# Performance work log

Hardware: AMD Instinct MI355X
Metric: run time of the kernel (lower is better)

Reference implementation:

```python
import jax, jax.numpy as jnp
import numpy as np

B, N, D = 4, 1024, 1024
H, DH = 16, 64
N_LAYERS = 3  # len(mlp_dims) - 1 with implicit_mlp_hiddens=(64, 64)
EPS = 1.1920929e-07  # torch.nn.RMSNorm default eps = finfo(float32).eps


def _rope_tables(n, dtype):
    # lucidrains RotaryEmbedding: theta=10000, interleaved freq repeat
    inv_freq = 1.0 / (10000.0 ** (np.arange(0, DH, 2, dtype=np.float64) / DH))
    t = np.arange(n, dtype=np.float64)[:, None] * inv_freq[None, :]  # [n, DH/2]
    t = np.repeat(t, 2, axis=-1)  # [n, DH], freqs interleaved (f0,f0,f1,f1,...)
    return jnp.asarray(np.cos(t), dtype), jnp.asarray(np.sin(t), dtype)


def _rope_rotate(x, cos, sin):
    # x: [b,h,n,d]; rotate_half on interleaved pairs: (x1,x2) -> (-x2,x1)
    xp = x.reshape(*x.shape[:-1], DH // 2, 2)
    xr = jnp.stack((-xp[..., 1], xp[..., 0]), axis=-1).reshape(x.shape)
    return x * cos + xr * sin


def _attend(q, k, v):
    # rotate_queries_with_cached_keys with no cache: same positions for q and k
    n = q.shape[-2]
    cos, sin = _rope_tables(n, q.dtype)
    q = _rope_rotate(q, cos, sin)
    k = _rope_rotate(k, cos, sin)
    scale = DH ** -0.5
    scores = jnp.einsum('bhqd,bhkd->bhqk', q, k) * scale
    causal = jnp.tril(jnp.ones((n, n), dtype=bool))
    scores = jnp.where(causal, scores, -jnp.inf)
    attn = jax.nn.softmax(scores, axis=-1)
    return jnp.einsum('bhqk,bhkd->bhqd', attn, v)


def _split_heads(x):
    b, n, _ = x.shape
    return x.reshape(b, n, H, DH).transpose(0, 2, 1, 3)  # b h n d


def setup_inputs() -> dict:
    key = jax.random.key(0)
    ks = jax.random.split(key, 6)
    s = 0.02
    return {
        'tokens': jax.random.normal(ks[0], (B, N, D), jnp.float32),
        'gamma': jnp.ones((D,), jnp.float32),                                  # RMSNorm weight
        'Wq': jax.random.normal(ks[1], (D, H * DH), jnp.float32) * s,           # to_queries
        'Wk': jax.random.normal(ks[2], (N_LAYERS, D, H * DH), jnp.float32) * s, # stacked key projections
        'Wv': jax.random.normal(ks[3], (N_LAYERS, D, H * DH), jnp.float32) * s, # stacked value projections
        'Wo': jax.random.normal(ks[4], (H * DH, D), jnp.float32) * s,           # to_out
    }


def reference(tokens, gamma, Wq, Wk, Wv, Wo):
    b, n, d = tokens.shape
    # RMSNorm (prenorm)
    x = tokens * jax.lax.rsqrt(jnp.mean(tokens * tokens, axis=-1, keepdims=True) + EPS) * gamma
    out = _split_heads(x @ Wq)  # queries, [b h n d]
    for i in range(N_LAYERS):
        k = _split_heads(x @ Wk[i])
        v = _split_heads(x @ Wv[i])
        out = _attend(out, k, v)
        if i < N_LAYERS - 1:
            out = jax.nn.silu(out)  # implicit MLP activation between attention stages
    out = out.transpose(0, 2, 1, 3).reshape(b, n, H * DH)  # merge heads
    return out @ Wo
```

## Files before the change

### kernel.cpp

```cpp
#include <hip/hip_runtime.h>


typedef unsigned short u16;
typedef short s16x8 __attribute__((ext_vector_type(8)));
typedef u16 u16x4 __attribute__((ext_vector_type(4)));
typedef float f32x4 __attribute__((ext_vector_type(4)));

typedef __attribute__((address_space(1))) const unsigned int as1c_uint;
typedef __attribute__((address_space(3))) unsigned int as3_uint;

__device__ __forceinline__ float b2f(u16 h) {
  union { unsigned int u; float f; } v; v.u = ((unsigned int)h) << 16; return v.f;
}
__device__ __forceinline__ u16 f2b(float f) {
  union { float f; unsigned int u; } v; v.f = f;
  return (u16)((v.u + 0x7FFFu + ((v.u >> 16) & 1u)) >> 16);
}
__device__ __forceinline__ void gload16(const u16* g, const u16* lds) {
  __builtin_amdgcn_global_load_lds((as1c_uint*)(size_t)g,
                                   (as3_uint*)(unsigned int)(size_t)lds, 16, 0, 0);
}

__global__ __launch_bounds__(256)
void rmsnorm_kernel(const float* __restrict__ T, const float* __restrict__ gamma,
                    u16* __restrict__ X) {
  const int row = blockIdx.x, tid = threadIdx.x;
  const float4 v = ((const float4*)(T + (size_t)row * 1024))[tid];
  float ss = v.x * v.x + v.y * v.y + v.z * v.z + v.w * v.w;
#pragma unroll
  for (int msk = 1; msk <= 32; msk <<= 1) ss += __shfl_xor(ss, msk, 64);
  __shared__ float red[4];
  if ((tid & 63) == 0) red[tid >> 6] = ss;
  __syncthreads();
  const float tot = red[0] + red[1] + red[2] + red[3];
  const float r = rsqrtf(tot * (1.0f / 1024.0f) + 1.1920929e-07f);
  const float4 gm = ((const float4*)gamma)[tid];
  u16x4 o;
  o[0] = f2b(v.x * r * gm.x); o[1] = f2b(v.y * r * gm.y);
  o[2] = f2b(v.z * r * gm.z); o[3] = f2b(v.w * r * gm.w);
  *(u16x4*)(X + (size_t)row * 1024 + tid * 4) = o;
}

__global__ __launch_bounds__(256)
void rope_kernel(float* __restrict__ ct, float* __restrict__ st) {
  const int idx = blockIdx.x * 256 + threadIdx.x;
  const int n = idx >> 5, j = idx & 31;
  const double freq = pow(10000.0, -(double)j / 32.0);
  const double a = (double)n * freq;
  ct[idx] = (float)cos(a);
  st[idx] = (float)sin(a);
}

__global__ __launch_bounds__(256)
void ropek_kernel(u16* __restrict__ K, const float* __restrict__ ct,
                  const float* __restrict__ st) {
  u16* row = K + (size_t)blockIdx.y * 4194304 + (size_t)blockIdx.x * 1024;
  const int n = blockIdx.x & 1023;
  const int t = threadIdx.x;
  const int j = ((t * 4) & 63) >> 1;
  const float2 c2 = *(const float2*)(ct + n * 32 + j);
  const float2 s2 = *(const float2*)(st + n * 32 + j);
  u16x4 v = *(u16x4*)(row + t * 4);
  const float x0 = b2f(v[0]), x1 = b2f(v[1]);
  const float y0 = b2f(v[2]), y1 = b2f(v[3]);
  u16x4 o;
  o[0] = f2b(x0 * c2.x - x1 * s2.x);
  o[1] = f2b(x1 * c2.x + x0 * s2.x);
  o[2] = f2b(y0 * c2.y - y1 * s2.y);
  o[3] = f2b(y1 * c2.y + y0 * s2.y);
  *(u16x4*)(row + t * 4) = o;
}

__global__ __launch_bounds__(256)
void transw_kernel(const float* __restrict__ Wq, const float* __restrict__ Wk,
                   const float* __restrict__ Wv, const float* __restrict__ Wo,
                   u16* __restrict__ wt) {
  __shared__ float tile[32][33];
  const int z = blockIdx.z;
  const float* src = (z == 0) ? Wq
                   : (z <= 3) ? (Wk + (size_t)(z - 1) * 1048576)
                   : (z <= 6) ? (Wv + (size_t)(z - 4) * 1048576)
                              : Wo;
  u16* dst = wt + (size_t)z * 1048576;
  const int tx = threadIdx.x & 31, ty = threadIdx.x >> 5;
  const int bx = blockIdx.x * 32, by = blockIdx.y * 32;
#pragma unroll
  for (int i = 0; i < 4; ++i)
    tile[ty + i * 8][tx] = src[(size_t)(by + ty + i * 8) * 1024 + bx + tx];
  __syncthreads();
#pragma unroll
  for (int i = 0; i < 4; ++i)
    dst[(size_t)(bx + ty + i * 8) * 1024 + by + tx] = f2b(tile[tx][ty + i * 8]);
}

template <int KIND>
__global__ __launch_bounds__(256)
void gemm_kernel(const u16* __restrict__ A, const u16* __restrict__ Bt,
                 void* __restrict__ Cout) {
  const int p = blockIdx.x;
  const int role = (p & 7) * (KIND == 0 ? 224 : 64) + (p >> 3);
  const int z = role >> 8;
  const int rem = role & 255;
  const int m0 = (rem >> 3) * 128;
  const int n0 = (rem & 7) * 128;

  const int tid = threadIdx.x;
  const int w = tid >> 6, l = tid & 63;
  const int g = l >> 4, ll = l & 15;
  const int wr = w >> 1, wc = w & 1;

  const u16* Ab;
  const u16* Bb;
  if (KIND == 0) {
    Ab = A + (size_t)m0 * 1024;
    Bb = Bt + (size_t)z * 1048576 + (size_t)n0 * 1024;
  } else {
    Ab = A + (size_t)m0 * 1024 + z * 512;
    Bb = Bt + (size_t)n0 * 1024 + z * 512;
  }

  __shared__ u16 SH[4][8192];

  const f32x4 zero = {0.f, 0.f, 0.f, 0.f};
  f32x4 acc[4][4];
#pragma unroll
  for (int i = 0; i < 4; ++i)
#pragma unroll
    for (int j = 0; j < 4; ++j) acc[i][j] = zero;

  auto stage = [&](int t2) {
    const int slot = t2 & 3;
    const int k0 = t2 * 32;
#pragma unroll
    for (int c = 0; c < 2; ++c) {
      const int chunk = c * 4 + w;
      const int row = chunk * 16 + (l >> 2);
      const int sl = l & 3;
      const int kk = k0 + ((sl ^ ((row >> 1) & 3)) << 3);
      gload16(Ab + (size_t)row * 1024 + kk, &SH[slot][chunk * 512]);
      gload16(Bb + (size_t)row * 1024 + kk, &SH[slot][4096 + chunk * 512]);
    }
  };

  const int NT = (KIND == 1) ? 16 : 32;
  stage(0); stage(1); stage(2);

#pragma unroll
  for (int t = 0; t < NT; ++t) {
    const int beyond = (NT - 1) - t;
    if (beyond >= 2)      asm volatile("s_waitcnt vmcnt(8)" ::: "memory");
    else if (beyond == 1) asm volatile("s_waitcnt vmcnt(4)" ::: "memory");
    else                  asm volatile("s_waitcnt vmcnt(0)" ::: "memory");
    __builtin_amdgcn_s_barrier();

    const int slot = t & 3;
    const u16* As = &SH[slot][0];
    const u16* Bs = &SH[slot][4096];
    s16x8 af[4], bfr[4];
#pragma unroll
    for (int mf = 0; mf < 4; ++mf) {
      const int row = wr * 64 + mf * 16 + ll;
      af[mf] = *(const s16x8*)&As[row * 32 + ((g ^ ((row >> 1) & 3)) << 3)];
    }
#pragma unroll
    for (int nf = 0; nf < 4; ++nf) {
      const int row = wc * 64 + nf * 16 + ll;
      bfr[nf] = *(const s16x8*)&Bs[row * 32 + ((g ^ ((row >> 1) & 3)) << 3)];
    }

    if (t + 3 < NT) stage(t + 3);

    __builtin_amdgcn_s_setprio(1);
#pragma unroll
    for (int mf = 0; mf < 4; ++mf)
#pragma unroll
      for (int nf = 0; nf < 4; ++nf)
        acc[mf][nf] = __builtin_amdgcn_mfma_f32_16x16x32_bf16(af[mf], bfr[nf],
                                                              acc[mf][nf], 0, 0, 0);
    __builtin_amdgcn_s_setprio(0);
  }
  __syncthreads();

  if (KIND == 0) {
    u16* C = (u16*)Cout + (size_t)z * 4194304;
    if (z < 4) {
      u16* T = &SH[0][0];
#pragma unroll
      for (int mf = 0; mf < 4; ++mf)
#pragma unroll
        for (int nf = 0; nf < 4; ++nf) {
          const int c = wc * 64 + nf * 16 + ll;
#pragma unroll
          for (int rg = 0; rg < 4; ++rg) {
            const int r = wr * 64 + mf * 16 + g * 4 + rg;
            T[r * 128 + (c ^ ((r & 7) << 4))] = f2b(acc[mf][nf][rg]);
          }
        }
      __syncthreads();
#pragma unroll
      for (int i = 0; i < 8; ++i) {
        const int R = (tid >> 4) + i * 16;
        const int c0 = (tid & 15) * 8;
        const s16x8 v = *(const s16x8*)&T[R * 128 + (c0 ^ ((R & 7) << 4))];
        *(s16x8*)&C[(size_t)(m0 + R) * 1024 + n0 + c0] = v;
      }
    } else {
#pragma unroll
      for (int mf = 0; mf < 4; ++mf)
#pragma unroll
        for (int nf = 0; nf < 4; ++nf) {
          const int col = n0 + wc * 64 + nf * 16 + ll;
          const int hh = col >> 6, d = col & 63;
          const int mb = m0 + wr * 64 + mf * 16 + g * 4;
          const int bb = mb >> 10, n = mb & 1023;
          u16x4 pk;
#pragma unroll
          for (int rg = 0; rg < 4; ++rg) pk[rg] = f2b(acc[mf][nf][rg]);
          *(u16x4*)&C[((size_t)((bb * 16 + hh) * 64 + d)) * 1024 + n] = pk;
        }
    }
  } else {
    float* C = (float*)Cout + (size_t)z * 4194304;
#pragma unroll
    for (int mf = 0; mf < 4; ++mf)
#pragma unroll
      for (int nf = 0; nf < 4; ++nf) {
        const int col = n0 + wc * 64 + nf * 16 + ll;
#pragma unroll
        for (int rg = 0; rg < 4; ++rg) {
          const int m = m0 + wr * 64 + mf * 16 + g * 4 + rg;
          C[(size_t)m * 1024 + col] = acc[mf][nf][rg];
        }
      }
  }
}

__global__ __launch_bounds__(256)
void reduce_kernel(const float* __restrict__ P, float* __restrict__ out) {
  const int i = (blockIdx.x * 256 + threadIdx.x) * 4;
  const float4 a = *(const float4*)(P + i);
  const float4 b = *(const float4*)(P + 4194304 + i);
  float4 o;
  o.x = a.x + b.x; o.y = a.y + b.y; o.z = a.z + b.z; o.w = a.w + b.w;
  *(float4*)(out + i) = o;
}

template <int SILU>
__global__ __launch_bounds__(256)
void attn_kernel(const u16* __restrict__ Q, const u16* __restrict__ K,
                 const u16* __restrict__ Vt, u16* __restrict__ O,
                 const float* __restrict__ ct, const float* __restrict__ st) {
  const int lin = blockIdx.x + (blockIdx.y << 3);
  const int role = (lin & 7) * 64 + (lin >> 3);
  const int p = role & 7, bh = role >> 3;
  const int q_lo = p, q_hi = 15 - p;
  const int b = bh >> 4, h = bh & 15;
  const int tid = threadIdx.x, w = tid >> 6, l = tid & 63;
  const int g = l >> 4, ll = l & 15;

  const u16* Qb = Q + (size_t)(b * 1024) * 1024 + h * 64;
  const u16* Kb = K + (size_t)(b * 1024) * 1024 + h * 64;
  const u16* Vb = Vt + (size_t)((b * 16 + h) * 64) * 1024;
  u16* Ob = O + (size_t)(b * 1024) * 1024 + h * 64;

  __shared__ u16 Ksh[2][64 * 72];
  __shared__ u16 Psh[4][16 * 72];

  s16x8 qfL[2], qfH[2];
  auto loadQ = [&](int qt, s16x8* qf) {
    const int qrow = qt * 64 + w * 16 + ll;
#pragma unroll
    for (int kc = 0; kc < 2; ++kc) {
      const int d0 = kc * 32 + g * 8;
      const int j0 = d0 >> 1;
      const float4 c4 = *(const float4*)(ct + qrow * 32 + j0);
      const float4 s4v = *(const float4*)(st + qrow * 32 + j0);
      const s16x8 qin = *(const s16x8*)(Qb + (size_t)qrow * 1024 + d0);
      s16x8 qo;
#pragma unroll
      for (int pp = 0; pp < 4; ++pp) {
        const float c = ((const float*)&c4)[pp], s = ((const float*)&s4v)[pp];
        const float x0 = b2f((u16)qin[2 * pp]), x1 = b2f((u16)qin[2 * pp + 1]);
        qo[2 * pp]     = (short)f2b((x0 * c - x1 * s) * 0.125f);
        qo[2 * pp + 1] = (short)f2b((x1 * c + x0 * s) * 0.125f);
      }
      qf[kc] = qo;
    }
  };
  loadQ(q_lo, qfL);
  loadQ(q_hi, qfH);

  float mL[4], lsL[4], mH[4], lsH[4];
  f32x4 oL[4], oH[4];
  const f32x4 zero = {0.f, 0.f, 0.f, 0.f};
#pragma unroll
  for (int rg = 0; rg < 4; ++rg) {
    mL[rg] = -3.0e38f; lsL[rg] = 0.f; mH[rg] = -3.0e38f; lsH[rg] = 0.f;
  }
#pragma unroll
  for (int df = 0; df < 4; ++df) { oL[df] = zero; oH[df] = zero; }

  const int srow = tid >> 2;
  const int sc0 = (tid & 3) * 16;

  s16x8 kr0, kr1;
  auto kload = [&](int t) {
    const u16* kp = Kb + (size_t)(t * 64 + srow) * 1024 + sc0;
    kr0 = *(const s16x8*)kp;
    kr1 = *(const s16x8*)(kp + 8);
  };
  auto kstore = [&](int bf) {
    *(s16x8*)&Ksh[bf][srow * 72 + sc0] = kr0;
    *(s16x8*)&Ksh[bf][srow * 72 + sc0 + 8] = kr1;
  };

  kload(0);
  kstore(0);
  __syncthreads();
  int buf = 0;

  for (int t = 0; t <= q_hi; ++t) {
    const bool pre = (t < q_hi);
    if (pre) kload(t + 1);

    s16x8 vb[2][4];
#pragma unroll
    for (int kc = 0; kc < 2; ++kc)
#pragma unroll
      for (int df = 0; df < 4; ++df)
        vb[kc][df] = *(const s16x8*)(Vb + (size_t)(df * 16 + ll) * 1024 +
                                     t * 64 + kc * 32 + g * 8);

    auto process = [&](const s16x8* qf, float* mm, float* ls, f32x4* o,
                       bool diag) {
      f32x4 s4[4];
      __builtin_amdgcn_s_setprio(1);
#pragma unroll
      for (int nf = 0; nf < 4; ++nf) {
        const s16x8 kb0 = *(const s16x8*)&Ksh[buf][(nf * 16 + ll) * 72 + g * 8];
        const s16x8 kb1 = *(const s16x8*)&Ksh[buf][(nf * 16 + ll) * 72 + 32 + g * 8];
        f32x4 sv = zero;
        sv = __builtin_amdgcn_mfma_f32_16x16x32_bf16(qf[0], kb0, sv, 0, 0, 0);
        sv = __builtin_amdgcn_mfma_f32_16x16x32_bf16(qf[1], kb1, sv, 0, 0, 0);
        s4[nf] = sv;
      }
      __builtin_amdgcn_s_setprio(0);

      if (diag) {
#pragma unroll
        for (int nf = 0; nf < 4; ++nf)
#pragma unroll
          for (int rg = 0; rg < 4; ++rg)
            if (nf * 16 + ll > w * 16 + g * 4 + rg) s4[nf][rg] = -3.0e38f;
      }

#pragma unroll
      for (int rg = 0; rg < 4; ++rg) {
        float rmax = fmaxf(fmaxf(s4[0][rg], s4[1][rg]),
                           fmaxf(s4[2][rg], s4[3][rg]));
        rmax = fmaxf(rmax, __shfl_xor(rmax, 1, 64));
        rmax = fmaxf(rmax, __shfl_xor(rmax, 2, 64));
        rmax = fmaxf(rmax, __shfl_xor(rmax, 4, 64));
        rmax = fmaxf(rmax, __shfl_xor(rmax, 8, 64));
        const float mn = fmaxf(mm[rg], rmax);
        const float scl = __expf(mm[rg] - mn);
        mm[rg] = mn;
        float ps = 0.f;
#pragma unroll
        for (int nf = 0; nf < 4; ++nf) {
          const float pv = __expf(s4[nf][rg] - mn);
          s4[nf][rg] = pv;
          ps += pv;
        }
        ls[rg] = ls[rg] * scl + ps;
#pragma unroll
        for (int df = 0; df < 4; ++df) o[df][rg] *= scl;
      }

#pragma unroll
      for (int nf = 0; nf < 4; ++nf)
#pragma unroll
        for (int rg = 0; rg < 4; ++rg)
          Psh[w][(g * 4 + rg) * 72 + nf * 16 + ll] = f2b(s4[nf][rg]);

      __builtin_amdgcn_s_setprio(1);
#pragma unroll
      for (int kc = 0; kc < 2; ++kc) {
        const s16x8 pa = *(const s16x8*)&Psh[w][ll * 72 + kc * 32 + g * 8];
#pragma unroll
        for (int df = 0; df < 4; ++df)
          o[df] = __builtin_amdgcn_mfma_f32_16x16x32_bf16(pa, vb[kc][df],
                                                          o[df], 0, 0, 0);
      }
      __builtin_amdgcn_s_setprio(0);
    };

    process(qfH, mH, lsH, oH, t == q_hi);
    if (t <= q_lo) process(qfL, mL, lsL, oL, t == q_lo);

    if (pre) kstore(buf ^ 1);
    __syncthreads();
    buf ^= 1;
  }

  auto finish = [&](float* ls, f32x4* o, int qt) {
#pragma unroll
    for (int rg = 0; rg < 4; ++rg) {
      float v = ls[rg];
      v += __shfl_xor(v, 1, 64);
      v += __shfl_xor(v, 2, 64);
      v += __shfl_xor(v, 4, 64);
      v += __shfl_xor(v, 8, 64);
      ls[rg] = 1.f / v;
    }
#pragma unroll
    for (int df = 0; df < 4; ++df)
#pragma unroll
      for (int rg = 0; rg < 4; ++rg) {
        float val = o[df][rg] * ls[rg];
        if (SILU) val = val / (1.f + __expf(-val));
        Ob[(size_t)(qt * 64 + w * 16 + g * 4 + rg) * 1024 + df * 16 + ll] =
            f2b(val);
      }
  };
  finish(lsH, oH, q_hi);
  finish(lsL, oL, q_lo);
}

extern "C" void kernel_launch(void* const* d_in, const int* in_sizes, int n_in,
                              void* d_out, int out_size, void* d_ws, size_t ws_size,
                              hipStream_t stream) {
  (void)in_sizes; (void)n_in; (void)out_size; (void)ws_size;
  const float* tokens = (const float*)d_in[0];
  const float* gamma  = (const float*)d_in[1];
  const float* Wq     = (const float*)d_in[2];
  const float* Wk     = (const float*)d_in[3];
  const float* Wv     = (const float*)d_in[4];
  const float* Wo     = (const float*)d_in[5];
  float* out = (float*)d_out;

  u16* x    = (u16*)d_ws;
  u16* wt   = x + (size_t)4096 * 1024;
  u16* qkv  = wt + (size_t)8 * 1048576;
  u16* outA = qkv + (size_t)7 * 4194304;
  u16* outB = outA + 4194304;
  float* ct = (float*)(outB + 4194304);
  float* st = ct + 32768;
  float* Pp = (float*)(qkv + 1 * 4194304);

  rmsnorm_kernel<<<4096, 256, 0, stream>>>(tokens, gamma, x);
  rope_kernel<<<128, 256, 0, stream>>>(ct, st);
  transw_kernel<<<dim3(32, 32, 8), 256, 0, stream>>>(Wq, Wk, Wv, Wo, wt);
  gemm_kernel<0><<<1792, 256, 0, stream>>>(x, wt, qkv);

  const size_t M4 = 4194304;
  ropek_kernel<<<dim3(4096, 3), 256, 0, stream>>>(qkv + M4, ct, st);

  attn_kernel<1><<<dim3(8, 64), 256, 0, stream>>>(qkv, qkv + 1 * M4, qkv + 4 * M4,
                                                  outA, ct, st);
  attn_kernel<1><<<dim3(8, 64), 256, 0, stream>>>(outA, qkv + 2 * M4, qkv + 5 * M4,
                                                  outB, ct, st);
  attn_kernel<0><<<dim3(8, 64), 256, 0, stream>>>(outB, qkv + 3 * M4, qkv + 6 * M4,
                                                  outA, ct, st);

  gemm_kernel<1><<<512, 256, 0, stream>>>(outA, wt + (size_t)7 * 1048576,
                                          (void*)Pp);
  reduce_kernel<<<4096, 256, 0, stream>>>(Pp, out);
}
```

Baseline: 239.5 us.

## Enlarge GEMM tile to 256x128 and split attention into one q-tile per block

The GEMM kernel's M-tile doubles to 256 rows, giving each wave 8x4 accumulators. It uses a 3-slot LDS pipeline instead of 4, and the grid is halved. The attention kernel drops the paired lo/hi q-tile balancing: each block handles a single 64-row query tile, the grid is doubled, and launch_bounds asks for 3 blocks per SM. The goals are more operand reuse in the GEMMs and more parallelism with fewer registers in attention, at the cost of uneven per-block work in the causal attention and higher register pressure in the GEMM.

```diff
diff --git a/kernel.cpp b/kernel.cpp
--- a/kernel.cpp
+++ b/kernel.cpp
@@ -94,14 +94,14 @@
 }
 
 template <int KIND>
-__global__ __launch_bounds__(256)
+__global__ __launch_bounds__(256, 2)
 void gemm_kernel(const u16* __restrict__ A, const u16* __restrict__ Bt,
                  void* __restrict__ Cout) {
   const int p = blockIdx.x;
-  const int role = (p & 7) * (KIND == 0 ? 224 : 64) + (p >> 3);
-  const int z = role >> 8;
-  const int rem = role & 255;
-  const int m0 = (rem >> 3) * 128;
+  const int role = (p & 7) * (KIND == 0 ? 112 : 32) + (p >> 3);
+  const int z = role >> 7;
+  const int rem = role & 127;
+  const int m0 = (rem >> 3) * 256;
   const int n0 = (rem & 7) * 128;
 
   const int tid = threadIdx.x;
@@ -119,60 +119,65 @@
     Bb = Bt + (size_t)n0 * 1024 + z * 512;
   }
 
-  __shared__ u16 SH[4][8192];
+  __shared__ u16 SH[3][12288];
 
   const f32x4 zero = {0.f, 0.f, 0.f, 0.f};
-  f32x4 acc[4][4];
-#pragma unroll
-  for (int i = 0; i < 4; ++i)
+  f32x4 acc[8][4];
+#pragma unroll
+  for (int i = 0; i < 8; ++i)
 #pragma unroll
     for (int j = 0; j < 4; ++j) acc[i][j] = zero;
 
   auto stage = [&](int t2) {
-    const int slot = t2 & 3;
+    const int slot = t2 % 3;
     const int k0 = t2 * 32;
+    const int rsub = l >> 2, sl = l & 3;
+#pragma unroll
+    for (int c = 0; c < 4; ++c) {
+      const int chunk = c * 4 + w;
+      const int row = chunk * 16 + rsub;
+      const int kk = k0 + ((sl ^ ((row >> 1) & 3)) << 3);
+      gload16(Ab + (size_t)row * 1024 + kk, &SH[slot][chunk * 512]);
+    }
 #pragma unroll
     for (int c = 0; c < 2; ++c) {
       const int chunk = c * 4 + w;
-      const int row = chunk * 16 + (l >> 2);
-      const int sl = l & 3;
+      const int row = chunk * 16 + rsub;
       const int kk = k0 + ((sl ^ ((row >> 1) & 3)) << 3);
-      gload16(Ab + (size_t)row * 1024 + kk, &SH[slot][chunk * 512]);
-      gload16(Bb + (size_t)row * 1024 + kk, &SH[slot][4096 + chunk * 512]);
+      gload16(Bb + (size_t)row * 1024 + kk, &SH[slot][8192 + chunk * 512]);
     }
   };
 
   const int NT = (KIND == 1) ? 16 : 32;
-  stage(0); stage(1); stage(2);
+  stage(0); stage(1);
 
 #pragma unroll
   for (int t = 0; t < NT; ++t) {
-    const int beyond = (NT - 1) - t;
-    if (beyond >= 2)      asm volatile("s_waitcnt vmcnt(8)" ::: "memory");
-    else if (beyond == 1) asm volatile("s_waitcnt vmcnt(4)" ::: "memory");
-    else                  asm volatile("s_waitcnt vmcnt(0)" ::: "memory");
+    if (t < NT - 1) asm volatile("s_waitcnt vmcnt(6)" ::: "memory");
+    else            asm volatile("s_waitcnt vmcnt(0)" ::: "memory");
     __builtin_amdgcn_s_barrier();
 
-    const int slot = t & 3;
+    const int slot = t % 3;
     const u16* As = &SH[slot][0];
-    const u16* Bs = &SH[slot][4096];
-    s16x8 af[4], bfr[4];
-#pragma unroll
-    for (int mf = 0; mf < 4; ++mf) {
-      const int row = wr * 64 + mf * 16 + ll;
-      af[mf] = *(const s16x8*)&As[row * 32 + ((g ^ ((row >> 1) & 3)) << 3)];
-    }
+    const u16* Bs = &SH[slot][8192];
+    s16x8 bfr[4];
 #pragma unroll
     for (int nf = 0; nf < 4; ++nf) {
       const int row = wc * 64 + nf * 16 + ll;
       bfr[nf] = *(const s16x8*)&Bs[row * 32 + ((g ^ ((row >> 1) & 3)) << 3)];
     }
-
-    if (t + 3 < NT) stage(t + 3);
+    s16x8 af[8];
+#pragma unroll
+    for (int mf = 0; mf < 8; ++mf) {
+      const int row = wr * 128 + mf * 16 + ll;
+      af[mf] = *(const s16x8*)&As[row * 32 + ((g ^ ((row >> 1) & 3)) << 3)];
+    }
+
+    if (t + 2 < NT) stage(t + 2);
 
     __builtin_amdgcn_s_setprio(1);
 #pragma unroll
-    for (int mf = 0; mf < 4; ++mf)
+    for (int mf = 0; mf < 8; ++mf)
 #pragma unroll
       for (int nf = 0; nf < 4; ++nf)
         acc[mf][nf] = __builtin_amdgcn_mfma_f32_16x16x32_bf16(af[mf], bfr[nf],
@@ -186,19 +191,19 @@
     if (z < 4) {
       u16* T = &SH[0][0];
 #pragma unroll
-      for (int mf = 0; mf < 4; ++mf)
+      for (int mf = 0; mf < 8; ++mf)
 #pragma unroll
         for (int nf = 0; nf < 4; ++nf) {
           const int c = wc * 64 + nf * 16 + ll;
 #pragma unroll
           for (int rg = 0; rg < 4; ++rg) {
-            const int r = wr * 64 + mf * 16 + g * 4 + rg;
+            const int r = wr * 128 + mf * 16 + g * 4 + rg;
             T[r * 128 + (c ^ ((r & 7) << 4))] = f2b(acc[mf][nf][rg]);
           }
         }
       __syncthreads();
 #pragma unroll
-      for (int i = 0; i < 8; ++i) {
+      for (int i = 0; i < 16; ++i) {
         const int R = (tid >> 4) + i * 16;
         const int c0 = (tid & 15) * 8;
         const s16x8 v = *(const s16x8*)&T[R * 128 + (c0 ^ ((R & 7) << 4))];
@@ -206,12 +211,12 @@
       }
     } else {
 #pragma unroll
-      for (int mf = 0; mf < 4; ++mf)
+      for (int mf = 0; mf < 8; ++mf)
 #pragma unroll
         for (int nf = 0; nf < 4; ++nf) {
           const int col = n0 + wc * 64 + nf * 16 + ll;
           const int hh = col >> 6, d = col & 63;
-          const int mb = m0 + wr * 64 + mf * 16 + g * 4;
+          const int mb = m0 + wr * 128 + mf * 16 + g * 4;
           const int bb = mb >> 10, n = mb & 1023;
           u16x4 pk;
 #pragma unroll
@@ -222,13 +227,13 @@
   } else {
     float* C = (float*)Cout + (size_t)z * 4194304;
 #pragma unroll
-    for (int mf = 0; mf < 4; ++mf)
+    for (int mf = 0; mf < 8; ++mf)
 #pragma unroll
       for (int nf = 0; nf < 4; ++nf) {
         const int col = n0 + wc * 64 + nf * 16 + ll;
 #pragma unroll
         for (int rg = 0; rg < 4; ++rg) {
-          const int m = m0 + wr * 64 + mf * 16 + g * 4 + rg;
+          const int m = m0 + wr * 128 + mf * 16 + g * 4 + rg;
           C[(size_t)m * 1024 + col] = acc[mf][nf][rg];
         }
       }
@@ -246,14 +251,14 @@
 }
 
 template <int SILU>
-__global__ __launch_bounds__(256)
+__global__ __launch_bounds__(256, 3)
 void attn_kernel(const u16* __restrict__ Q, const u16* __restrict__ K,
                  const u16* __restrict__ Vt, u16* __restrict__ O,
                  const float* __restrict__ ct, const float* __restrict__ st) {
-  const int lin = blockIdx.x + (blockIdx.y << 3);
-  const int role = (lin & 7) * 64 + (lin >> 3);
-  const int p = role & 7, bh = role >> 3;
-  const int q_lo = p, q_hi = 15 - p;
+  const int lin = blockIdx.x + (blockIdx.y << 4);
+  const int role = (lin & 7) * 128 + (lin >> 3);
+  const int bh = role >> 4;
+  const int qt = 15 - (role & 15);
   const int b = bh >> 4, h = bh & 15;
   const int tid = threadIdx.x, w = tid >> 6, l = tid & 63;
   const int g = l >> 4, ll = l & 15;
@@ -266,39 +271,33 @@
   __shared__ u16 Ksh[2][64 * 72];
   __shared__ u16 Psh[4][16 * 72];
 
-  s16x8 qfL[2], qfH[2];
-  auto loadQ = [&](int qt, s16x8* qf) {
-    const int qrow = qt * 64 + w * 16 + ll;
-#pragma unroll
-    for (int kc = 0; kc < 2; ++kc) {
-      const int d0 = kc * 32 + g * 8;
-      const int j0 = d0 >> 1;
-      const float4 c4 = *(const float4*)(ct + qrow * 32 + j0);
-      const float4 s4v = *(const float4*)(st + qrow * 32 + j0);
-      const s16x8 qin = *(const s16x8*)(Qb + (size_t)qrow * 1024 + d0);
-      s16x8 qo;
-#pragma unroll
-      for (int pp = 0; pp < 4; ++pp) {
-        const float c = ((const float*)&c4)[pp], s = ((const float*)&s4v)[pp];
-        const float x0 = b2f((u16)qin[2 * pp]), x1 = b2f((u16)qin[2 * pp + 1]);
-        qo[2 * pp]     = (short)f2b((x0 * c - x1 * s) * 0.125f);
-        qo[2 * pp + 1] = (short)f2b((x1 * c + x0 * s) * 0.125f);
-      }
-      qf[kc] = qo;
-    }
-  };
-  loadQ(q_lo, qfL);
-  loadQ(q_hi, qfH);
-
-  float mL[4], lsL[4], mH[4], lsH[4];
-  f32x4 oL[4], oH[4];
+  const int qrow = qt * 64 + w * 16 + ll;
+  s16x8 qf[2];
+#pragma unroll
+  for (int kc = 0; kc < 2; ++kc) {
+    const int d0 = kc * 32 + g * 8;
+    const int j0 = d0 >> 1;
+    const float4 c4 = *(const float4*)(ct + qrow * 32 + j0);
+    const float4 s4v = *(const float4*)(st + qrow * 32 + j0);
+    const s16x8 qin = *(const s16x8*)(Qb + (size_t)qrow * 1024 + d0);
+    s16x8 qo;
+#pragma unroll
+    for (int pp = 0; pp < 4; ++pp) {
+      const float c = ((const float*)&c4)[pp], s = ((const float*)&s4v)[pp];
+      const float x0 = b2f((u16)qin[2 * pp]), x1 = b2f((u16)qin[2 * pp + 1]);
+      qo[2 * pp]     = (short)f2b((x0 * c - x1 * s) * 0.125f);
+      qo[2 * pp + 1] = (short)f2b((x1 * c + x0 * s) * 0.125f);
+    }
+    qf[kc] = qo;
+  }
+
+  float m[4], lsum[4];
+  f32x4 o[4];
   const f32x4 zero = {0.f, 0.f, 0.f, 0.f};
 #pragma unroll
-  for (int rg = 0; rg < 4; ++rg) {
-    mL[rg] = -3.0e38f; lsL[rg] = 0.f; mH[rg] = -3.0e38f; lsH[rg] = 0.f;
-  }
-#pragma unroll
-  for (int df = 0; df < 4; ++df) { oL[df] = zero; oH[df] = zero; }
+  for (int rg = 0; rg < 4; ++rg) { m[rg] = -3.0e38f; lsum[rg] = 0.f; }
+#pragma unroll
+  for (int df = 0; df < 4; ++df) o[df] = zero;
 
   const int srow = tid >> 2;
   const int sc0 = (tid & 3) * 16;
@@ -319,8 +318,8 @@
   __syncthreads();
   int buf = 0;
 
-  for (int t = 0; t <= q_hi; ++t) {
-    const bool pre = (t < q_hi);
+  for (int t = 0; t <= qt; ++t) {
+    const bool pre = (t < qt);
     if (pre) kload(t + 1);
 
     s16x8 vb[2][4];
@@ -331,100 +330,90 @@
         vb[kc][df] = *(const s16x8*)(Vb + (size_t)(df * 16 + ll) * 1024 +
                                      t * 64 + kc * 32 + g * 8);
 
-    auto process = [&](const s16x8* qf, float* mm, float* ls, f32x4* o,
-                       bool diag) {
-      f32x4 s4[4];
-      __builtin_amdgcn_s_setprio(1);
+    f32x4 s4[4];
+    __builtin_amdgcn_s_setprio(1);
+#pragma unroll
+    for (int nf = 0; nf < 4; ++nf) {
+      const s16x8 kb0 = *(const s16x8*)&Ksh[buf][(nf * 16 + ll) * 72 + g * 8];
+      const s16x8 kb1 = *(const s16x8*)&Ksh[buf][(nf * 16 + ll) * 72 + 32 + g * 8];
+      f32x4 sv = zero;
+      sv = __builtin_amdgcn_mfma_f32_16x16x32_bf16(qf[0], kb0, sv, 0, 0, 0);
+      sv = __builtin_amdgcn_mfma_f32_16x16x32_bf16(qf[1], kb1, sv, 0, 0, 0);
+      s4[nf] = sv;
+    }
+    __builtin_amdgcn_s_setprio(0);
+
+    if (t == qt) {
+#pragma unroll
+      for (int nf = 0; nf < 4; ++nf)
+#pragma unroll
+        for (int rg = 0; rg < 4; ++rg)
+          if (nf * 16 + ll > w * 16 + g * 4 + rg) s4[nf][rg] = -3.0e38f;
+    }
+
+#pragma unroll
+    for (int rg = 0; rg < 4; ++rg) {
+      float rmax = fmaxf(fmaxf(s4[0][rg], s4[1][rg]),
+                         fmaxf(s4[2][rg], s4[3][rg]));
+      rmax = fmaxf(rmax, __shfl_xor(rmax, 1, 64));
+      rmax = fmaxf(rmax, __shfl_xor(rmax, 2, 64));
+      rmax = fmaxf(rmax, __shfl_xor(rmax, 4, 64));
+      rmax = fmaxf(rmax, __shfl_xor(rmax, 8, 64));
+      const float mn = fmaxf(m[rg], rmax);
+      const float scl = __expf(m[rg] - mn);
+      m[rg] = mn;
+      float ps = 0.f;
 #pragma unroll
       for (int nf = 0; nf < 4; ++nf) {
-        const s16x8 kb0 = *(const s16x8*)&Ksh[buf][(nf * 16 + ll) * 72 + g * 8];
-        const s16x8 kb1 = *(const s16x8*)&Ksh[buf][(nf * 16 + ll) * 72 + 32 + g * 8];
-        f32x4 sv = zero;
-        sv = __builtin_amdgcn_mfma_f32_16x16x32_bf16(qf[0], kb0, sv, 0, 0, 0);
-        sv = __builtin_amdgcn_mfma_f32_16x16x32_bf16(qf[1], kb1, sv, 0, 0, 0);
-        s4[nf] = sv;
+        const float pv = __expf(s4[nf][rg] - mn);
+        s4[nf][rg] = pv;
+        ps += pv;
       }
-      __builtin_amdgcn_s_setprio(0);
-
-      if (diag) {
-#pragma unroll
-        for (int nf = 0; nf < 4; ++nf)
-#pragma unroll
-          for (int rg = 0; rg < 4; ++rg)
-            if (nf * 16 + ll > w * 16 + g * 4 + rg) s4[nf][rg] = -3.0e38f;
-      }
-
-#pragma unroll
-      for (int rg = 0; rg < 4; ++rg) {
-        float rmax = fmaxf(fmaxf(s4[0][rg], s4[1][rg]),
-                           fmaxf(s4[2][rg], s4[3][rg]));
-        rmax = fmaxf(rmax, __shfl_xor(rmax, 1, 64));
-        rmax = fmaxf(rmax, __shfl_xor(rmax, 2, 64));
-        rmax = fmaxf(rmax, __shfl_xor(rmax, 4, 64));
-        rmax = fmaxf(rmax, __shfl_xor(rmax, 8, 64));
-        const float mn = fmaxf(mm[rg], rmax);
-        const float scl = __expf(mm[rg] - mn);
-        mm[rg] = mn;
-        float ps = 0.f;
-#pragma unroll
-        for (int nf = 0; nf < 4; ++nf) {
-          const float pv = __expf(s4[nf][rg] - mn);
-          s4[nf][rg] = pv;
-          ps += pv;
-        }
-        ls[rg] = ls[rg] * scl + ps;
-#pragma unroll
-        for (int df = 0; df < 4; ++df) o[df][rg] *= scl;
-      }
-
-#pragma unroll
-      for (int nf = 0; nf < 4; ++nf)
-#pragma unroll
-        for (int rg = 0; rg < 4; ++rg)
-          Psh[w][(g * 4 + rg) * 72 + nf * 16 + ll] = f2b(s4[nf][rg]);
-
-      __builtin_amdgcn_s_setprio(1);
-#pragma unroll
-      for (int kc = 0; kc < 2; ++kc) {
-        const s16x8 pa = *(const s16x8*)&Psh[w][ll * 72 + kc * 32 + g * 8];
-#pragma unroll
-        for (int df = 0; df < 4; ++df)
-          o[df] = __builtin_amdgcn_mfma_f32_16x16x32_bf16(pa, vb[kc][df],
-                                                          o[df], 0, 0, 0);
-      }
-      __builtin_amdgcn_s_setprio(0);
-    };
-
-    process(qfH, mH, lsH, oH, t == q_hi);
-    if (t <= q_lo) process(qfL, mL, lsL, oL, t == q_lo);
+      lsum[rg] = lsum[rg] * scl + ps;
+#pragma unroll
+      for (int df = 0; df < 4; ++df) o[df][rg] *= scl;
+    }
+
+#pragma unroll
+    for (int nf = 0; nf < 4; ++nf)
+#pragma unroll
+      for (int rg = 0; rg < 4; ++rg)
+        Psh[w][(g * 4 + rg) * 72 + nf * 16 + ll] = f2b(s4[nf][rg]);
+
+    __builtin_amdgcn_s_setprio(1);
+#pragma unroll
+    for (int kc = 0; kc < 2; ++kc) {
+      const s16x8 pa = *(const s16x8*)&Psh[w][ll * 72 + kc * 32 + g * 8];
+#pragma unroll
+      for (int df = 0; df < 4; ++df)
+        o[df] = __builtin_amdgcn_mfma_f32_16x16x32_bf16(pa, vb[kc][df],
+                                                        o[df], 0, 0, 0);
+    }
+    __builtin_amdgcn_s_setprio(0);
 
     if (pre) kstore(buf ^ 1);
     __syncthreads();
     buf ^= 1;
   }
 
-  auto finish = [&](float* ls, f32x4* o, int qt) {
+#pragma unroll
+  for (int rg = 0; rg < 4; ++rg) {
+    float v = lsum[rg];
+    v += __shfl_xor(v, 1, 64);
+    v += __shfl_xor(v, 2, 64);
+    v += __shfl_xor(v, 4, 64);
+    v += __shfl_xor(v, 8, 64);
+    lsum[rg] = 1.f / v;
+  }
+#pragma unroll
+  for (int df = 0; df < 4; ++df)
 #pragma unroll
     for (int rg = 0; rg < 4; ++rg) {
-      float v = ls[rg];
-      v += __shfl_xor(v, 1, 64);
-      v += __shfl_xor(v, 2, 64);
-      v += __shfl_xor(v, 4, 64);
-      v += __shfl_xor(v, 8, 64);
-      ls[rg] = 1.f / v;
-    }
-#pragma unroll
-    for (int df = 0; df < 4; ++df)
-#pragma unroll
-      for (int rg = 0; rg < 4; ++rg) {
-        float val = o[df][rg] * ls[rg];
-        if (SILU) val = val / (1.f + __expf(-val));
-        Ob[(size_t)(qt * 64 + w * 16 + g * 4 + rg) * 1024 + df * 16 + ll] =
-            f2b(val);
-      }
-  };
-  finish(lsH, oH, q_hi);
-  finish(lsL, oL, q_lo);
+      float val = o[df][rg] * lsum[rg];
+      if (SILU) val = val / (1.f + __expf(-val));
+      Ob[(size_t)(qt * 64 + w * 16 + g * 4 + rg) * 1024 + df * 16 + ll] =
+          f2b(val);
+    }
 }
 
 extern "C" void kernel_launch(void* const* d_in, const int* in_sizes, int n_in,
@@ -451,19 +440,19 @@
   rmsnorm_kernel<<<4096, 256, 0, stream>>>(tokens, gamma, x);
   rope_kernel<<<128, 256, 0, stream>>>(ct, st);
   transw_kernel<<<dim3(32, 32, 8), 256, 0, stream>>>(Wq, Wk, Wv, Wo, wt);
-  gemm_kernel<0><<<1792, 256, 0, stream>>>(x, wt, qkv);
+  gemm_kernel<0><<<896, 256, 0, stream>>>(x, wt, qkv);
 
   const size_t M4 = 4194304;
   ropek_kernel<<<dim3(4096, 3), 256, 0, stream>>>(qkv + M4, ct, st);
 
-  attn_kernel<1><<<dim3(8, 64), 256, 0, stream>>>(qkv, qkv + 1 * M4, qkv + 4 * M4,
-                                                  outA, ct, st);
-  attn_kernel<1><<<dim3(8, 64), 256, 0, stream>>>(outA, qkv + 2 * M4, qkv + 5 * M4,
-                                                  outB, ct, st);
-  attn_kernel<0><<<dim3(8, 64), 256, 0, stream>>>(outB, qkv + 3 * M4, qkv + 6 * M4,
-                                                  outA, ct, st);
-
-  gemm_kernel<1><<<512, 256, 0, stream>>>(outA, wt + (size_t)7 * 1048576,
+  attn_kernel<1><<<dim3(16, 64), 256, 0, stream>>>(qkv, qkv + 1 * M4, qkv + 4 * M4,
+                                                   outA, ct, st);
+  attn_kernel<1><<<dim3(16, 64), 256, 0, stream>>>(outA, qkv + 2 * M4, qkv + 5 * M4,
+                                                   outB, ct, st);
+  attn_kernel<0><<<dim3(16, 64), 256, 0, stream>>>(outB, qkv + 3 * M4, qkv + 6 * M4,
+                                                   outA, ct, st);
+
+  gemm_kernel<1><<<256, 256, 0, stream>>>(outA, wt + (size_t)7 * 1048576,
                                           (void*)Pp);
   reduce_kernel<<<4096, 256, 0, stream>>>(Pp, out);
 }
```

Measured after the change: 291.0 us. +21.5%, slower.

## Fuse key RoPE into QKV GEMM epilogue and enlarge M tile

Applied to the files above, without the earlier changes.

Removes the separate ropek kernel and applies the rotary rotation to the K projections inside the QKV GEMM's LDS-staged epilogue. This saves one read-modify-write pass over three K tensors plus a launch. The QKV GEMM tile grows to 256x128 (MB=8), which halves the block count. The pipeline drops from a 4-slot, 3-deep prefetch to 3 slots, 2 deep, with launch bounds requesting 2 blocks per CU. The bigger tile raises register pressure (acc[8][4]) and cuts latency hiding, so it may lose occupancy.

```diff
diff --git a/kernel.cpp b/kernel.cpp
--- a/kernel.cpp
+++ b/kernel.cpp
@@ -49,26 +49,6 @@
   const double a = (double)n * freq;
   ct[idx] = (float)cos(a);
   st[idx] = (float)sin(a);
-}
-
-__global__ __launch_bounds__(256)
-void ropek_kernel(u16* __restrict__ K, const float* __restrict__ ct,
-                  const float* __restrict__ st) {
-  u16* row = K + (size_t)blockIdx.y * 4194304 + (size_t)blockIdx.x * 1024;
-  const int n = blockIdx.x & 1023;
-  const int t = threadIdx.x;
-  const int j = ((t * 4) & 63) >> 1;
-  const float2 c2 = *(const float2*)(ct + n * 32 + j);
-  const float2 s2 = *(const float2*)(st + n * 32 + j);
-  u16x4 v = *(u16x4*)(row + t * 4);
-  const float x0 = b2f(v[0]), x1 = b2f(v[1]);
-  const float y0 = b2f(v[2]), y1 = b2f(v[3]);
-  u16x4 o;
-  o[0] = f2b(x0 * c2.x - x1 * s2.x);
-  o[1] = f2b(x1 * c2.x + x0 * s2.x);
-  o[2] = f2b(y0 * c2.y - y1 * s2.y);
-  o[3] = f2b(y1 * c2.y + y0 * s2.y);
-  *(u16x4*)(row + t * 4) = o;
 }
 
 __global__ __launch_bounds__(256)
@@ -94,14 +74,19 @@
 }
 
 template <int KIND>
-__global__ __launch_bounds__(256)
+__global__ __launch_bounds__(256, 2)
 void gemm_kernel(const u16* __restrict__ A, const u16* __restrict__ Bt,
-                 void* __restrict__ Cout) {
+                 void* __restrict__ Cout, const float* __restrict__ ct,
+                 const float* __restrict__ st) {
+  constexpr int MB = (KIND == 0) ? 8 : 4;
+  constexpr int BM = MB * 32;
+  constexpr int ASLOT = BM * 32;
+  constexpr int SLOT = (BM + 128) * 32;
   const int p = blockIdx.x;
-  const int role = (p & 7) * (KIND == 0 ? 224 : 64) + (p >> 3);
-  const int z = role >> 8;
-  const int rem = role & 255;
-  const int m0 = (rem >> 3) * 128;
+  const int role = (p & 7) * (KIND == 0 ? 112 : 64) + (p >> 3);
+  const int z = (KIND == 0) ? (role >> 7) : (role >> 8);
+  const int rem = (KIND == 0) ? (role & 127) : (role & 255);
+  const int m0 = (rem >> 3) * BM;
   const int n0 = (rem & 7) * 128;
 
   const int tid = threadIdx.x;
@@ -119,60 +104,69 @@
     Bb = Bt + (size_t)n0 * 1024 + z * 512;
   }
 
-  __shared__ u16 SH[4][8192];
+  __shared__ u16 SH[3][SLOT];
 
   const f32x4 zero = {0.f, 0.f, 0.f, 0.f};
-  f32x4 acc[4][4];
-#pragma unroll
-  for (int i = 0; i < 4; ++i)
+  f32x4 acc[MB][4];
+#pragma unroll
+  for (int i = 0; i < MB; ++i)
 #pragma unroll
     for (int j = 0; j < 4; ++j) acc[i][j] = zero;
 
   auto stage = [&](int t2) {
-    const int slot = t2 & 3;
+    const int slot = t2 % 3;
     const int k0 = t2 * 32;
+    const int rsub = l >> 2, sl = l & 3;
+#pragma unroll
+    for (int c = 0; c < MB / 2; ++c) {
+      const int chunk = c * 4 + w;
+      const int row = chunk * 16 + rsub;
+      const int kk = k0 + ((sl ^ ((row >> 1) & 3)) << 3);
+      gload16(Ab + (size_t)row * 1024 + kk, &SH[slot][chunk * 512]);
+    }
 #pragma unroll
     for (int c = 0; c < 2; ++c) {
       const int chunk = c * 4 + w;
-      const int row = chunk * 16 + (l >> 2);
-      const int sl = l & 3;
+      const int row = chunk * 16 + rsub;
       const int kk = k0 + ((sl ^ ((row >> 1) & 3)) << 3);
-      gload16(Ab + (size_t)row * 1024 + kk, &SH[slot][chunk * 512]);
-      gload16(Bb + (size_t)row * 1024 + kk, &SH[slot][4096 + chunk * 512]);
+      gload16(Bb + (size_t)row * 1024 + kk, &SH[slot][ASLOT + chunk * 512]);
     }
   };
 
   const int NT = (KIND == 1) ? 16 : 32;
-  stage(0); stage(1); stage(2);
+  stage(0); stage(1);
 
 #pragma unroll
   for (int t = 0; t < NT; ++t) {
-    const int beyond = (NT - 1) - t;
-    if (beyond >= 2)      asm volatile("s_waitcnt vmcnt(8)" ::: "memory");
-    else if (beyond == 1) asm volatile("s_waitcnt vmcnt(4)" ::: "memory");
-    else                  asm volatile("s_waitcnt vmcnt(0)" ::: "memory");
+    if (t < NT - 1) {
+      if constexpr (KIND == 0) asm volatile("s_waitcnt vmcnt(6)" ::: "memory");
+      else                     asm volatile("s_waitcnt vmcnt(4)" ::: "memory");
+    } else {
+      asm volatile("s_waitcnt vmcnt(0)" ::: "memory");
+    }
     __builtin_amdgcn_s_barrier();
 
-    const int slot = t & 3;
+    const int slot = t % 3;
     const u16* As = &SH[slot][0];
-    const u16* Bs = &SH[slot][4096];
-    s16x8 af[4], bfr[4];
-#pragma unroll
-    for (int mf = 0; mf < 4; ++mf) {
-      const int row = wr * 64 + mf * 16 + ll;
-      af[mf] = *(const s16x8*)&As[row * 32 + ((g ^ ((row >> 1) & 3)) << 3)];
-    }
+    const u16* Bs = &SH[slot][ASLOT];
+    s16x8 bfr[4];
 #pragma unroll
     for (int nf = 0; nf < 4; ++nf) {
       const int row = wc * 64 + nf * 16 + ll;
       bfr[nf] = *(const s16x8*)&Bs[row * 32 + ((g ^ ((row >> 1) & 3)) << 3)];
     }
-
-    if (t + 3 < NT) stage(t + 3);
+    s16x8 af[MB];
+#pragma unroll
+    for (int mf = 0; mf < MB; ++mf) {
+      const int row = wr * (MB * 16) + mf * 16 + ll;
+      af[mf] = *(const s16x8*)&As[row * 32 + ((g ^ ((row >> 1) & 3)) << 3)];
+    }
+
+    if (t + 2 < NT) stage(t + 2);
 
     __builtin_amdgcn_s_setprio(1);
 #pragma unroll
-    for (int mf = 0; mf < 4; ++mf)
+    for (int mf = 0; mf < MB; ++mf)
 #pragma unroll
       for (int nf = 0; nf < 4; ++nf)
         acc[mf][nf] = __builtin_amdgcn_mfma_f32_16x16x32_bf16(af[mf], bfr[nf],
@@ -184,34 +178,51 @@
   if (KIND == 0) {
     u16* C = (u16*)Cout + (size_t)z * 4194304;
     if (z < 4) {
+      const bool doRope = (z >= 1);
       u16* T = &SH[0][0];
 #pragma unroll
-      for (int mf = 0; mf < 4; ++mf)
+      for (int mf = 0; mf < MB; ++mf)
 #pragma unroll
         for (int nf = 0; nf < 4; ++nf) {
           const int c = wc * 64 + nf * 16 + ll;
 #pragma unroll
           for (int rg = 0; rg < 4; ++rg) {
-            const int r = wr * 64 + mf * 16 + g * 4 + rg;
+            const int r = wr * (MB * 16) + mf * 16 + g * 4 + rg;
             T[r * 128 + (c ^ ((r & 7) << 4))] = f2b(acc[mf][nf][rg]);
           }
         }
       __syncthreads();
 #pragma unroll
-      for (int i = 0; i < 8; ++i) {
+      for (int i = 0; i < BM / 16; ++i) {
         const int R = (tid >> 4) + i * 16;
         const int c0 = (tid & 15) * 8;
-        const s16x8 v = *(const s16x8*)&T[R * 128 + (c0 ^ ((R & 7) << 4))];
+        s16x8 v = *(const s16x8*)&T[R * 128 + (c0 ^ ((R & 7) << 4))];
+        if (doRope) {
+          const int n = (m0 + R) & 1023;
+          const int j0 = (c0 & 63) >> 1;
+          const float4 c4 = *(const float4*)(ct + n * 32 + j0);
+          const float4 s4 = *(const float4*)(st + n * 32 + j0);
+          s16x8 vo;
+#pragma unroll
+          for (int pp = 0; pp < 4; ++pp) {
+            const float c = ((const float*)&c4)[pp];
+            const float s = ((const float*)&s4)[pp];
+            const float x0 = b2f((u16)v[2 * pp]), x1 = b2f((u16)v[2 * pp + 1]);
+            vo[2 * pp]     = (short)f2b(x0 * c - x1 * s);
+            vo[2 * pp + 1] = (short)f2b(x1 * c + x0 * s);
+          }
+          v = vo;
+        }
         *(s16x8*)&C[(size_t)(m0 + R) * 1024 + n0 + c0] = v;
       }
     } else {
 #pragma unroll
-      for (int mf = 0; mf < 4; ++mf)
+      for (int mf = 0; mf < MB; ++mf)
 #pragma unroll
         for (int nf = 0; nf < 4; ++nf) {
           const int col = n0 + wc * 64 + nf * 16 + ll;
           const int hh = col >> 6, d = col & 63;
-          const int mb = m0 + wr * 64 + mf * 16 + g * 4;
+          const int mb = m0 + wr * (MB * 16) + mf * 16 + g * 4;
           const int bb = mb >> 10, n = mb & 1023;
           u16x4 pk;
 #pragma unroll
@@ -222,13 +233,13 @@
   } else {
     float* C = (float*)Cout + (size_t)z * 4194304;
 #pragma unroll
-    for (int mf = 0; mf < 4; ++mf)
+    for (int mf = 0; mf < MB; ++mf)
 #pragma unroll
       for (int nf = 0; nf < 4; ++nf) {
         const int col = n0 + wc * 64 + nf * 16 + ll;
 #pragma unroll
         for (int rg = 0; rg < 4; ++rg) {
-          const int m = m0 + wr * 64 + mf * 16 + g * 4 + rg;
+          const int m = m0 + wr * (MB * 16) + mf * 16 + g * 4 + rg;
           C[(size_t)m * 1024 + col] = acc[mf][nf][rg];
         }
       }
@@ -451,11 +462,9 @@
   rmsnorm_kernel<<<4096, 256, 0, stream>>>(tokens, gamma, x);
   rope_kernel<<<128, 256, 0, stream>>>(ct, st);
   transw_kernel<<<dim3(32, 32, 8), 256, 0, stream>>>(Wq, Wk, Wv, Wo, wt);
-  gemm_kernel<0><<<1792, 256, 0, stream>>>(x, wt, qkv);
+  gemm_kernel<0><<<896, 256, 0, stream>>>(x, wt, qkv, ct, st);
 
   const size_t M4 = 4194304;
-  ropek_kernel<<<dim3(4096, 3), 256, 0, stream>>>(qkv + M4, ct, st);
-
   attn_kernel<1><<<dim3(8, 64), 256, 0, stream>>>(qkv, qkv + 1 * M4, qkv + 4 * M4,
                                                   outA, ct, st);
   attn_kernel<1><<<dim3(8, 64), 256, 0, stream>>>(outA, qkv + 2 * M4, qkv + 5 * M4,
@@ -464,6 +473,6 @@
                                                   outA, ct, st);
 
   gemm_kernel<1><<<512, 256, 0, stream>>>(outA, wt + (size_t)7 * 1048576,
-                                          (void*)Pp);
+                                          (void*)Pp, ct, st);
   reduce_kernel<<<4096, 256, 0, stream>>>(Pp, out);
 }
```

Result: faster. 229.8 us (-4.0%).
